# Performance work log

Hardware: AMD Instinct MI355X
Metric: run time of the kernel (lower is better)

The kernel has to match this reference:

```python
import jax, jax.numpy as jnp
import numpy as np

B, N, F = 32, 1024, 128

def setup_inputs() -> dict:
    key = jax.random.key(0)
    k1, k2, k3, k4 = jax.random.split(key, 4)
    adjMs = jax.random.uniform(k1, (B, N, N), dtype=jnp.float32)
    feats = jax.random.normal(k2, (B, N, F), dtype=jnp.float32)
    w = jax.random.normal(k3, (F, F), dtype=jnp.float32) * 0.05  # random_normal init scale
    b = jax.random.normal(k4, (1,), dtype=jnp.float32)
    return {"adjMs": adjMs, "feats": feats, "w": w, "b": b}

def reference(adjMs, feats, w, b):
    # adj[b,i,j] = feats[b,i] @ w @ feats[b,j] + b  (bilinear form V W V^T + b)
    vw = jnp.einsum('bnf,fg->bng', feats, w)          # [B,N,F]
    y = jnp.einsum('bng,bmg->bnm', vw, feats) + b[0]  # [B,N,N]
    # activation = 'linear' (identity); invertProb=False so no inversion branch
    return (y, feats)
```

## Files before the change

### kernel.cpp

```cpp
#include <hip/hip_runtime.h>

#define Bsz 32
#define Nn  1024
#define Ff  128

typedef __attribute__((ext_vector_type(8))) short bf16x8;
typedef __attribute__((ext_vector_type(4))) float f32x4;

static __device__ inline short f2bf(float f) {
    unsigned u = __builtin_bit_cast(unsigned, f);
    unsigned r = u + 0x7FFFu + ((u >> 16) & 1u);
    return (short)(r >> 16);
}

__global__ __launch_bounds__(256) void k0_wt(
    const float* __restrict__ w, short* __restrict__ wT)
{
    int gid = blockIdx.x * blockDim.x + threadIdx.x;
    if (gid < Ff * Ff) {
        int g = gid >> 7, k = gid & 127;
        wT[gid] = f2bf(w[k * Ff + g]);
    }
}

__global__ __launch_bounds__(256) void k1_fused(
    const float* __restrict__ feats,
    const short* __restrict__ wT,
    float* __restrict__ out_feats,
    short* __restrict__ fb,
    short* __restrict__ vw)
{
    const int row0 = blockIdx.x * 64;
    const int tid  = threadIdx.x;
    const int wid  = tid >> 6;
    const int lane = tid & 63;
    const int lr = lane & 15;
    const int kg = lane >> 4;

    const int myrow = row0 + wid * 16 + lr;
    const float* frow = feats + (size_t)myrow * Ff;
    float* orow       = out_feats + (size_t)myrow * Ff;
    short* brow       = fb + (size_t)myrow * Ff;

    f32x4 acc[8] = {};

    for (int kc = 0; kc < 4; ++kc) {
        int k0 = kc * 32 + kg * 8;
        float4 v0 = ((const float4*)(frow + k0))[0];
        float4 v1 = ((const float4*)(frow + k0))[1];
        ((float4*)(orow + k0))[0] = v0;
        ((float4*)(orow + k0))[1] = v1;
        bf16x8 a = (bf16x8){ f2bf(v0.x), f2bf(v0.y), f2bf(v0.z), f2bf(v0.w),
                             f2bf(v1.x), f2bf(v1.y), f2bf(v1.z), f2bf(v1.w) };
        *((bf16x8*)(brow + k0)) = a;
        for (int nf = 0; nf < 8; ++nf) {
            bf16x8 b = *((const bf16x8*)(wT + (size_t)(nf * 16 + lr) * Ff + k0));
            acc[nf] = __builtin_amdgcn_mfma_f32_16x16x32_bf16(a, b, acc[nf], 0, 0, 0);
        }
    }

    for (int nf = 0; nf < 8; ++nf) {
        int g = nf * 16 + lr;
        for (int r = 0; r < 4; ++r)
            vw[(size_t)(row0 + wid * 16 + kg * 4 + r) * Ff + g] = f2bf(acc[nf][r]);
    }
}

__global__ __launch_bounds__(256) void gemm2_kernel(
    const short* __restrict__ vw,
    const short* __restrict__ fb,
    const float* __restrict__ bias,
    float* __restrict__ y)
{
    int blk   = blockIdx.x;
    int xcd   = blk & 7;
    int q     = blk >> 3;
    int chunk = q >> 4;
    int k     = q & 15;
    int super_id = chunk * 8 + xcd;
    int bidx  = super_id >> 2;
    int s     = super_id & 3;
    int sm = s >> 1, sn = s & 1;
    int mt = sm * 4 + (k >> 2);
    int nt = sn * 4 + (k & 3);

    int tid = threadIdx.x;
    int wid = tid >> 6, lane = tid & 63;
    int wm = wid >> 1, wn = wid & 1;
    int lr = lane & 15, kg = lane >> 4;

    const short* A  = vw + (size_t)bidx * Nn * Ff;
    const short* Bp = fb + (size_t)bidx * Nn * Ff;
    int am0 = mt * 128 + wm * 64;
    int bn0 = nt * 128 + wn * 64;

    f32x4 acc[4][4] = {};

    for (int kc = 0; kc < 4; ++kc) {
        int k0 = kc * 32 + kg * 8;
        bf16x8 a[4], b[4];
        for (int mf = 0; mf < 4; ++mf)
            a[mf] = *((const bf16x8*)(A + (size_t)(am0 + mf * 16 + lr) * Ff + k0));
        for (int nf = 0; nf < 4; ++nf)
            b[nf] = *((const bf16x8*)(Bp + (size_t)(bn0 + nf * 16 + lr) * Ff + k0));
        for (int mf = 0; mf < 4; ++mf)
            for (int nf = 0; nf < 4; ++nf)
                acc[mf][nf] = __builtin_amdgcn_mfma_f32_16x16x32_bf16(
                    a[mf], b[nf], acc[mf][nf], 0, 0, 0);
    }

    float bv = bias[0];
    float* Y = y + (size_t)bidx * Nn * Nn;
    for (int mf = 0; mf < 4; ++mf) {
        int row = am0 + mf * 16 + kg * 4;
        for (int nf = 0; nf < 4; ++nf) {
            int col = bn0 + nf * 16 + lr;
            float* p = Y + (size_t)row * Nn + col;
            for (int r = 0; r < 4; ++r)
                p[(size_t)r * Nn] = acc[mf][nf][r] + bv;
        }
    }
}

extern "C" void kernel_launch(void* const* d_in, const int* in_sizes, int n_in,
                              void* d_out, int out_size, void* d_ws, size_t ws_size,
                              hipStream_t stream) {
    const float* feats = (const float*)d_in[1];
    const float* w     = (const float*)d_in[2];
    const float* bias  = (const float*)d_in[3];
    float* y = (float*)d_out;
    float* out_feats = y + (size_t)Bsz * Nn * Nn;

    short* vw = (short*)d_ws;
    short* fb = vw + (size_t)Bsz * Nn * Ff;
    short* wT = fb + (size_t)Bsz * Nn * Ff;

    k0_wt<<<64, 256, 0, stream>>>(w, wT);
    k1_fused<<<512, 256, 0, stream>>>(feats, wT, out_feats, fb, vw);
    gemm2_kernel<<<2048, 256, 0, stream>>>(vw, fb, bias, y);
}
```

Baseline: 65.44 us.

## Fuse weight transpose into first GEMM via swizzled LDS, add nontemporal stores

```diff
diff --git a/kernel.cpp b/kernel.cpp
--- a/kernel.cpp
+++ b/kernel.cpp
@@ -12,50 +12,66 @@
     unsigned r = u + 0x7FFFu + ((u >> 16) & 1u);
     return (short)(r >> 16);
 }
-
-__global__ __launch_bounds__(256) void k0_wt(
-    const float* __restrict__ w, short* __restrict__ wT)
-{
-    int gid = blockIdx.x * blockDim.x + threadIdx.x;
-    if (gid < Ff * Ff) {
-        int g = gid >> 7, k = gid & 127;
-        wT[gid] = f2bf(w[k * Ff + g]);
-    }
+static __device__ inline unsigned pack2(float lo, float hi) {
+    return (unsigned)(unsigned short)f2bf(lo) | ((unsigned)(unsigned short)f2bf(hi) << 16);
 }
 
-__global__ __launch_bounds__(256) void k1_fused(
+__global__ __launch_bounds__(256) void k1_fused_wt(
     const float* __restrict__ feats,
-    const short* __restrict__ wT,
+    const float* __restrict__ w,
     float* __restrict__ out_feats,
     short* __restrict__ fb,
     short* __restrict__ vw)
 {
-    const int row0 = blockIdx.x * 64;
+    __shared__ short wT_lds[128 * 128];
+
     const int tid  = threadIdx.x;
     const int wid  = tid >> 6;
     const int lane = tid & 63;
     const int lr = lane & 15;
     const int kg = lane >> 4;
 
+    {
+        const int g    = tid >> 1;
+        const int kb   = (tid & 1) * 64;
+        const int swzg = (g & 7) << 4;
+        const size_t gofs = (size_t)g;
+        for (int kk = 0; kk < 64; kk += 2) {
+            int k = kb + kk;
+            float lo = w[(size_t)k * Ff + gofs];
+            float hi = w[(size_t)(k + 1) * Ff + gofs];
+            unsigned pk = pack2(lo, hi);
+            *(unsigned*)((char*)wT_lds + (g << 8) + ((k * 2) ^ swzg)) = pk;
+        }
+    }
+
+    const int row0  = blockIdx.x * 64;
     const int myrow = row0 + wid * 16 + lr;
     const float* frow = feats + (size_t)myrow * Ff;
     float* orow       = out_feats + (size_t)myrow * Ff;
     short* brow       = fb + (size_t)myrow * Ff;
 
-    f32x4 acc[8] = {};
-
+    bf16x8 a[4];
     for (int kc = 0; kc < 4; ++kc) {
         int k0 = kc * 32 + kg * 8;
-        float4 v0 = ((const float4*)(frow + k0))[0];
-        float4 v1 = ((const float4*)(frow + k0))[1];
-        ((float4*)(orow + k0))[0] = v0;
-        ((float4*)(orow + k0))[1] = v1;
-        bf16x8 a = (bf16x8){ f2bf(v0.x), f2bf(v0.y), f2bf(v0.z), f2bf(v0.w),
-                             f2bf(v1.x), f2bf(v1.y), f2bf(v1.z), f2bf(v1.w) };
-        *((bf16x8*)(brow + k0)) = a;
+        f32x4 v0 = ((const f32x4*)(frow + k0))[0];
+        f32x4 v1 = ((const f32x4*)(frow + k0))[1];
+        __builtin_nontemporal_store(v0, (f32x4*)(orow + k0));
+        __builtin_nontemporal_store(v1, (f32x4*)(orow + k0) + 1);
+        a[kc] = (bf16x8){ f2bf(v0[0]), f2bf(v0[1]), f2bf(v0[2]), f2bf(v0[3]),
+                          f2bf(v1[0]), f2bf(v1[1]), f2bf(v1[2]), f2bf(v1[3]) };
+        *((bf16x8*)(brow + k0)) = a[kc];
+    }
+    __syncthreads();
+
+    f32x4 acc[8] = {};
+    const int swz = (lr & 7) << 4;
+    for (int kc = 0; kc < 4; ++kc) {
+        const int kbyte = kc * 64 + kg * 16;
         for (int nf = 0; nf < 8; ++nf) {
-            bf16x8 b = *((const bf16x8*)(wT + (size_t)(nf * 16 + lr) * Ff + k0));
-            acc[nf] = __builtin_amdgcn_mfma_f32_16x16x32_bf16(a, b, acc[nf], 0, 0, 0);
+            const int row = nf * 16 + lr;
+            bf16x8 b = *(const bf16x8*)((char*)wT_lds + (row << 8) + (kbyte ^ swz));
+            acc[nf] = __builtin_amdgcn_mfma_f32_16x16x32_bf16(a[kc], b, acc[nf], 0, 0, 0);
         }
     }
 
@@ -117,7 +133,7 @@
             int col = bn0 + nf * 16 + lr;
             float* p = Y + (size_t)row * Nn + col;
             for (int r = 0; r < 4; ++r)
-                p[(size_t)r * Nn] = acc[mf][nf][r] + bv;
+                __builtin_nontemporal_store(acc[mf][nf][r] + bv, p + (size_t)r * Nn);
         }
     }
 }
@@ -133,9 +149,7 @@
 
     short* vw = (short*)d_ws;
     short* fb = vw + (size_t)Bsz * Nn * Ff;
-    short* wT = fb + (size_t)Bsz * Nn * Ff;
 
-    k0_wt<<<64, 256, 0, stream>>>(w, wT);
-    k1_fused<<<512, 256, 0, stream>>>(feats, wT, out_feats, fb, vw);
+    k1_fused_wt<<<512, 256, 0, stream>>>(feats, w, out_feats, fb, vw);
     gemm2_kernel<<<2048, 256, 0, stream>>>(vw, fb, bias, y);
 }
```

Measured after the change: 65.25 us. No clear change (-0.3%).
